# Kernel optimization log

Measured on AMD Instinct MI355X. Metric: run time of the kernel, lower is better.

The kernel has to match this reference:

```python
import jax, jax.numpy as jnp
import numpy as np

N = 100000
E = 3200000
NUM_FEATURES = 32
SEQ_LEN = 12


def setup_inputs() -> dict:
    key = jax.random.key(0)
    ks = jax.random.split(key, 32)
    x = jax.random.normal(ks[0], (N, NUM_FEATURES), dtype=jnp.float32)
    edge_index = jax.random.randint(ks[1], (2, E), 0, N, dtype=jnp.int64)

    def lin(k, fan_in, fan_out):
        k1, k2 = jax.random.split(k)
        s = 1.0 / np.sqrt(fan_in)
        W = jax.random.uniform(k1, (fan_in, fan_out), jnp.float32, -s, s)
        b = jax.random.uniform(k2, (fan_out,), jnp.float32, -s, s)
        return W, b

    W_fp, b_fp = lin(ks[2], NUM_FEATURES, 64)   # feature_proj
    W1, b1 = lin(ks[3], 64, 64)                 # conv1
    W2, b2 = lin(ks[4], 64, 32)                 # conv2
    W3, b3 = lin(ks[5], 32, 16)                 # conv3
    W_tp, b_tp = lin(ks[6], 1, 16)              # temporal_proj

    def lstm_params(k, in_dim, hid):
        k1, k2, k3, k4 = jax.random.split(k, 4)
        s = 1.0 / np.sqrt(hid)
        Wih = jax.random.uniform(k1, (4 * hid, in_dim), jnp.float32, -s, s)
        Whh = jax.random.uniform(k2, (4 * hid, hid), jnp.float32, -s, s)
        bih = jax.random.uniform(k3, (4 * hid,), jnp.float32, -s, s)
        bhh = jax.random.uniform(k4, (4 * hid,), jnp.float32, -s, s)
        return Wih, Whh, bih, bhh

    Wih0, Whh0, bih0, bhh0 = lstm_params(ks[7], 16, 32)
    Wih1, Whh1, bih1, bhh1 = lstm_params(ks[8], 32, 32)
    W_fc1, b_fc1 = lin(ks[9], 32, 16)
    W_fc2, b_fc2 = lin(ks[10], 16, 1)

    return dict(x=x, edge_index=edge_index,
                W_fp=W_fp, b_fp=b_fp, W1=W1, b1=b1, W2=W2, b2=b2, W3=W3, b3=b3,
                W_tp=W_tp, b_tp=b_tp,
                Wih0=Wih0, Whh0=Whh0, bih0=bih0, bhh0=bhh0,
                Wih1=Wih1, Whh1=Whh1, bih1=bih1, bhh1=bhh1,
                W_fc1=W_fc1, b_fc1=b_fc1, W_fc2=W_fc2, b_fc2=b_fc2)


def _gcn_conv(h, W, b, src, dst, norm, n_nodes):
    # PyG GCNConv: transform then D^-1/2 (A+I) D^-1/2 aggregation, bias after
    h = h @ W                                   # [N, out]
    msg = h[src] * norm[:, None]                # gather + scale  [E+N, out]
    out = jax.ops.segment_sum(msg, dst, num_segments=n_nodes)
    return out + b


def _lstm_layer(x_tnd, Wih, Whh, bih, bhh):
    # x_tnd: [T, N, in]; PyTorch gate order i, f, g, o
    n, hid = x_tnd.shape[1], Whh.shape[1]
    h0 = jnp.zeros((n, hid), x_tnd.dtype)
    c0 = jnp.zeros((n, hid), x_tnd.dtype)
    pre_x = jnp.einsum('tnd,gd->tng', x_tnd, Wih) + (bih + bhh)

    def step(carry, px):
        h, c = carry
        g = px + h @ Whh.T
        i, f, gg, o = jnp.split(g, 4, axis=-1)
        i = jax.nn.sigmoid(i); f = jax.nn.sigmoid(f)
        gg = jnp.tanh(gg); o = jax.nn.sigmoid(o)
        c = f * c + i * gg
        h = o * jnp.tanh(c)
        return (h, c), h

    (_, _), hs = jax.lax.scan(step, (h0, c0), pre_x)
    return hs  # [T, N, hid]


def reference(x, edge_index, W_fp, b_fp, W1, b1, W2, b2, W3, b3, W_tp, b_tp,
              Wih0, Whh0, bih0, bhh0, Wih1, Whh1, bih1, bhh1,
              W_fc1, b_fc1, W_fc2, b_fc2):
    n_nodes = x.shape[0]
    # edge filtering is a no-op here (all indices in [0, N)); add self-loops
    loops = jnp.arange(n_nodes, dtype=edge_index.dtype)
    src = jnp.concatenate([edge_index[0], loops])
    dst = jnp.concatenate([edge_index[1], loops])
    deg = jax.ops.segment_sum(jnp.ones_like(dst, dtype=x.dtype), dst,
                              num_segments=n_nodes)
    dinv = jnp.where(deg > 0, jax.lax.rsqrt(deg), 0.0)
    norm = dinv[src] * dinv[dst]

    h = jax.nn.relu(x @ W_fp + b_fp)
    h = jax.nn.relu(_gcn_conv(h, W1, b1, src, dst, norm, n_nodes))
    h = jax.nn.relu(_gcn_conv(h, W2, b2, src, dst, norm, n_nodes))
    h = jax.nn.relu(_gcn_conv(h, W3, b3, src, dst, norm, n_nodes))
    # NOTE: per the original forward, h (GCN output) is discarded below.
    _ = h

    temporal = x[:, -SEQ_LEN:].reshape(n_nodes, SEQ_LEN, 1)
    temporal = temporal @ W_tp + b_tp                 # [N, T, 16]
    t = jnp.transpose(temporal, (1, 0, 2))            # [T, N, 16]
    t = _lstm_layer(t, Wih0, Whh0, bih0, bhh0)
    t = _lstm_layer(t, Wih1, Whh1, bih1, bhh1)
    last = t[-1]                                      # [N, 32]
    out = jax.nn.relu(last @ W_fc1 + b_fc1) @ W_fc2 + b_fc2
    return out
```

## Files before the change

### kernel.cpp

```cpp
#include <hip/hip_runtime.h>

#define NN   100000
#define SEQ  12
#define NPB  48
#define XSTR 64
#define RSTR 384
#define GRID ((NN + NPB - 1) / NPB)

typedef float f32x4 __attribute__((ext_vector_type(4)));
typedef short s16x8 __attribute__((ext_vector_type(8)));

#define OFF_U    0
#define OFF_V    2048
#define OFF_B1F  4096
#define OFF_FC1  6144
#define OFF_BFC1 6656
#define OFF_FC2  6672
#define OFF_BFC2 6688
#define OFF_A    6720

#define L2E  1.4426950408889634f
#define L2E2 2.8853900817779268f

#if defined(__has_builtin)
#if __has_builtin(__builtin_amdgcn_exp2f)
#define EXP2(x) __builtin_amdgcn_exp2f(x)
#endif
#endif
#ifndef EXP2
#define EXP2(x) exp2f(x)
#endif

__device__ __forceinline__ float rcp_fast(float v) { return __builtin_amdgcn_rcpf(v); }
__device__ __forceinline__ float sigm_p(float a) { return rcp_fast(1.0f + EXP2(a)); }
__device__ __forceinline__ float tanh_p(float a) {
    return fmaf(-2.0f, rcp_fast(1.0f + EXP2(a)), 1.0f);
}
__device__ __forceinline__ unsigned short f2bf(float f) {
    unsigned u = __float_as_uint(f);
    u = u + 0x7FFFu + ((u >> 16) & 1u);
    return (unsigned short)(u >> 16);
}
__device__ __forceinline__ float bf2f(unsigned short h) {
    return __uint_as_float(((unsigned)h) << 16);
}
__device__ __forceinline__ void hsplit(float h, unsigned& uh, unsigned& ul) {
    asm("v_cvt_pk_bf16_f32 %0, %1, %1" : "=v"(uh) : "v"(h));
    const float lo = h - __uint_as_float(uh << 16);
    asm("v_cvt_pk_bf16_f32 %0, %1, %1" : "=v"(ul) : "v"(lo));
}

#define MF(a, b, c) __builtin_amdgcn_mfma_f32_16x16x32_bf16((a), (b), (c), 0, 0, 0)

__global__ void repack(const float* __restrict__ Wtp,  const float* __restrict__ btp,
                       const float* __restrict__ Wih0, const float* __restrict__ Whh0,
                       const float* __restrict__ bih0, const float* __restrict__ bhh0,
                       const float* __restrict__ Wih1, const float* __restrict__ Whh1,
                       const float* __restrict__ bih1, const float* __restrict__ bhh1,
                       const float* __restrict__ Wfc1, const float* __restrict__ bfc1,
                       const float* __restrict__ Wfc2, const float* __restrict__ bfc2,
                       float* __restrict__ ws)
{
    const int tid = threadIdx.x;
    for (int idx = tid; idx < 2048; idx += 256) {
        int tau = idx >> 8, lane = (idx >> 2) & 63, reg = idx & 3;
        int grow = 16 * tau + (lane >> 4) * 4 + reg;
        int k = grow >> 2, g = grow & 3;
        int orig = g * 32 + k;
        float sg = (g == 2) ? L2E2 : -L2E;
        float u = 0.f, v = 0.f;
        for (int d = 0; d < 16; ++d) {
            u = fmaf(Wih0[orig * 16 + d], Wtp[d], u);
            v = fmaf(Wih0[orig * 16 + d], btp[d], v);
        }
        ws[OFF_U + idx]   = sg * u;
        ws[OFF_V + idx]   = sg * (v + bih0[orig] + bhh0[orig]);
        ws[OFF_B1F + idx] = sg * (bih1[orig] + bhh1[orig]);
    }
    short* wsS = (short*)(ws + OFF_A);
    for (int idx = tid; idx < 8192; idx += 256) {
        int tau = idx >> 10, t = (idx >> 9) & 1, lane = (idx >> 3) & 63, e = idx & 7;
        int rl = lane & 15, g = rl & 3;
        int orig = g * 32 + 4 * tau + (rl >> 2);
        int j = (lane >> 4) * 8 + e;
        float sg = (g == 2) ? L2E2 : -L2E;
        float f = sg * Whh0[orig * 32 + j];
        unsigned short hi = f2bf(f);
        wsS[idx] = (short)(t == 0 ? hi : f2bf(f - bf2f(hi)));
    }
    for (int idx = tid; idx < 16384; idx += 256) {
        int tau = idx >> 11, kap = (idx >> 10) & 1, t = (idx >> 9) & 1;
        int lane = (idx >> 3) & 63, e = idx & 7;
        int rl = lane & 15, g = rl & 3;
        int orig = g * 32 + 4 * tau + (rl >> 2);
        int j = (lane >> 4) * 8 + e;
        float sg = (g == 2) ? L2E2 : -L2E;
        float f = sg * (kap ? Whh1[orig * 32 + j] : Wih1[orig * 32 + j]);
        unsigned short hi = f2bf(f);
        wsS[8192 + idx] = (short)(t == 0 ? hi : f2bf(f - bf2f(hi)));
    }
    for (int idx = tid; idx < 512; idx += 256) {
        int m = idx >> 5, j = idx & 31;
        ws[OFF_FC1 + idx] = Wfc1[j * 16 + m];
    }
    if (tid < 16) { ws[OFF_BFC1 + tid] = bfc1[tid]; ws[OFF_FC2 + tid] = Wfc2[tid]; }
    if (tid == 0) ws[OFF_BFC2] = bfc2[0];
}

template<int P>
__device__ __forceinline__ void lstm_step(
    short* __restrict__ B0, short* __restrict__ B1,
    const float*& sxp, float* __restrict__ fin,
    f32x4 uf, f32x4 vf, f32x4 b1f,
    s16x8 A0h, s16x8 A0l, s16x8 A10h, s16x8 A10l, s16x8 A11h, s16x8 A11l,
    float (&c0)[3], float (&c1)[3],
    int col, int lg, int ku, bool last)
{
    constexpr int NP = P ^ 1;
    const int nb = col * 8;
    const short* rb0 = B0 + lg * RSTR + nb;
    const short* rb1 = B1 + lg * RSTR + nb;
    short* wb0 = B0 + (ku >> 3) * RSTR + nb + (ku & 7);
    short* wb1 = B1 + (ku >> 3) * RSTR + nb + (ku & 7);

#pragma unroll
    for (int i = 0; i < 3; ++i) {
        const float xv = sxp[i * 16];
        f32x4 acc = { fmaf(uf[0], xv, vf[0]), fmaf(uf[1], xv, vf[1]),
                      fmaf(uf[2], xv, vf[2]), fmaf(uf[3], xv, vf[3]) };
        const s16x8 bh = *(const s16x8*)(rb0 + (P * 8) * RSTR + i * 128);
        const s16x8 bl = *(const s16x8*)(rb0 + (P * 8 + 4) * RSTR + i * 128);
        acc = MF(A0h, bh, acc);
        acc = MF(A0l, bh, acc);
        acc = MF(A0h, bl, acc);
        const float gi = sigm_p(acc[0]);
        const float gf = sigm_p(acc[1]);
        const float gg = tanh_p(acc[2]);
        const float go = sigm_p(acc[3]);
        const float cc = fmaf(gf, c0[i], gi * gg);
        c0[i] = cc;
        const float h = go * tanh_p(L2E2 * cc);
        unsigned uh, ul; hsplit(h, uh, ul);
        wb0[(NP * 8) * RSTR + i * 128]     = (short)uh;
        wb0[(NP * 8 + 4) * RSTR + i * 128] = (short)ul;
    }
    __syncthreads();

#pragma unroll
    for (int i = 0; i < 3; ++i) {
        f32x4 acc = { b1f[0], b1f[1], b1f[2], b1f[3] };
        const s16x8 b0h = *(const s16x8*)(rb0 + (NP * 8) * RSTR + i * 128);
        const s16x8 b0l = *(const s16x8*)(rb0 + (NP * 8 + 4) * RSTR + i * 128);
        const s16x8 b1h = *(const s16x8*)(rb1 + (P * 8) * RSTR + i * 128);
        const s16x8 b1l = *(const s16x8*)(rb1 + (P * 8 + 4) * RSTR + i * 128);
        acc = MF(A10h, b0h, acc);
        acc = MF(A10l, b0h, acc);
        acc = MF(A10h, b0l, acc);
        acc = MF(A11h, b1h, acc);
        acc = MF(A11l, b1h, acc);
        acc = MF(A11h, b1l, acc);
        const float gi = sigm_p(acc[0]);
        const float gf = sigm_p(acc[1]);
        const float gg = tanh_p(acc[2]);
        const float go = sigm_p(acc[3]);
        const float cc = fmaf(gf, c1[i], gi * gg);
        c1[i] = cc;
        const float h = go * tanh_p(L2E2 * cc);
        if (last) {
            fin[ku * NPB + col + i * 16] = h;
        } else {
            unsigned uh, ul; hsplit(h, uh, ul);
            wb1[(NP * 8) * RSTR + i * 128]     = (short)uh;
            wb1[(NP * 8 + 4) * RSTR + i * 128] = (short)ul;
        }
    }
    sxp += XSTR;
}

__global__ __launch_bounds__(512)
void lstm_mfma(const float* __restrict__ x, const float* __restrict__ ws,
               float* __restrict__ out)
{
    __shared__ short sB[2 * 16 * RSTR];
    __shared__ float sx[SEQ][XSTR];

    const int tid  = threadIdx.x;
    const int lane = tid & 63;
    const int w    = __builtin_amdgcn_readfirstlane(tid >> 6);
    const int lg   = lane >> 4, col = lane & 15;
    const int ku   = 4 * w + lg;
    const int b0   = blockIdx.x * NPB;

    for (int i = tid; i < SEQ * XSTR; i += 512) {
        int t = i >> 6, nd = i & (XSTR - 1);
        int n = b0 + nd;
        sx[t][nd] = (nd < NPB && n < NN) ? x[(size_t)n * 32 + 20 + t] : 0.f;
    }
    int* z = (int*)sB;
    for (int i = tid; i < 16 * RSTR; i += 512) z[i] = 0;

    const f32x4 uf  = *(const f32x4*)(ws + OFF_U   + (w * 64 + lane) * 4);
    const f32x4 vf  = *(const f32x4*)(ws + OFF_V   + (w * 64 + lane) * 4);
    const f32x4 b1f = *(const f32x4*)(ws + OFF_B1F + (w * 64 + lane) * 4);
    const short* AS  = (const short*)(ws + OFF_A);
    const s16x8 A0h  = *(const s16x8*)(AS + ((w * 2 + 0) * 64 + lane) * 8);
    const s16x8 A0l  = *(const s16x8*)(AS + ((w * 2 + 1) * 64 + lane) * 8);
    const short* AS1 = AS + 8192;
    const s16x8 A10h = *(const s16x8*)(AS1 + ((w * 4 + 0) * 64 + lane) * 8);
    const s16x8 A10l = *(const s16x8*)(AS1 + ((w * 4 + 1) * 64 + lane) * 8);
    const s16x8 A11h = *(const s16x8*)(AS1 + ((w * 4 + 2) * 64 + lane) * 8);
    const s16x8 A11l = *(const s16x8*)(AS1 + ((w * 4 + 3) * 64 + lane) * 8);

    short* B0 = sB;
    short* B1 = sB + 16 * RSTR;
    float* fin = (float*)(B0 + 8 * RSTR);

    float c0[3], c1[3];
#pragma unroll
    for (int i = 0; i < 3; ++i) { c0[i] = 0.f; c1[i] = 0.f; }

    __syncthreads();

    const float* sxp = &sx[0][0] + col;
#pragma unroll 1
    for (int tt = 0; tt < SEQ / 2; ++tt) {
        lstm_step<0>(B0, B1, sxp, fin, uf, vf, b1f,
                     A0h, A0l, A10h, A10l, A11h, A11l,
                     c0, c1, col, lg, ku, false);
        lstm_step<1>(B0, B1, sxp, fin, uf, vf, b1f,
                     A0h, A0l, A10h, A10l, A11h, A11l,
                     c0, c1, col, lg, ku, tt == SEQ / 2 - 1);
    }

    __syncthreads();

    if (w == 0 && lane < NPB) {
        const int nd = lane;
        float acc2 = ws[OFF_BFC2];
#pragma unroll
        for (int m = 0; m < 16; ++m) {
            const float* fp = ws + OFF_FC1 + m * 32;
            float y = ws[OFF_BFC1 + m];
#pragma unroll
            for (int j = 0; j < 32; ++j)
                y = fmaf(fp[j], fin[j * NPB + nd], y);
            acc2 = fmaf(fmaxf(y, 0.f), ws[OFF_FC2 + m], acc2);
        }
        if (b0 + nd < NN) out[b0 + nd] = acc2;
    }
}

extern "C" void kernel_launch(void* const* d_in, const int* in_sizes, int n_in,
                              void* d_out, int out_size, void* d_ws, size_t ws_size,
                              hipStream_t stream) {
    (void)in_sizes; (void)n_in; (void)out_size; (void)ws_size;
    const float* x    = (const float*)d_in[0];
    const float* Wtp  = (const float*)d_in[10];
    const float* btp  = (const float*)d_in[11];
    const float* Wih0 = (const float*)d_in[12];
    const float* Whh0 = (const float*)d_in[13];
    const float* bih0 = (const float*)d_in[14];
    const float* bhh0 = (const float*)d_in[15];
    const float* Wih1 = (const float*)d_in[16];
    const float* Whh1 = (const float*)d_in[17];
    const float* bih1 = (const float*)d_in[18];
    const float* bhh1 = (const float*)d_in[19];
    const float* Wfc1 = (const float*)d_in[20];
    const float* bfc1 = (const float*)d_in[21];
    const float* Wfc2 = (const float*)d_in[22];
    const float* bfc2 = (const float*)d_in[23];
    float* ws  = (float*)d_ws;
    float* out = (float*)d_out;

    hipLaunchKernelGGL(repack, dim3(1), dim3(256), 0, stream,
                       Wtp, btp, Wih0, Whh0, bih0, bhh0,
                       Wih1, Whh1, bih1, bhh1, Wfc1, bfc1, Wfc2, bfc2, ws);
    hipLaunchKernelGGL(lstm_mfma, dim3(GRID), dim3(512), 0, stream,
                       x, ws, out);
}
```

Measured before the change: 141.2 us.

## Halve block to 4 waves, each wave computing two gate tiles

Each block now runs 256 threads instead of 512. Every wave handles two of the eight 16-unit hidden tiles, so it holds two sets of weight fragments, biases and cell states in registers. The layer-1 MFMAs for the two tiles are interleaved so the shared B-fragment loads are reused. This targets lower barrier cost, more instruction-level parallelism per wave and fewer redundant LDS B loads, at the cost of higher register pressure and fewer waves per block to hide latency.

```diff
diff --git a/kernel.cpp b/kernel.cpp
--- a/kernel.cpp
+++ b/kernel.cpp
@@ -111,73 +111,95 @@
 __device__ __forceinline__ void lstm_step(
     short* __restrict__ B0, short* __restrict__ B1,
     const float*& sxp, float* __restrict__ fin,
-    f32x4 uf, f32x4 vf, f32x4 b1f,
-    s16x8 A0h, s16x8 A0l, s16x8 A10h, s16x8 A10l, s16x8 A11h, s16x8 A11l,
-    float (&c0)[3], float (&c1)[3],
-    int col, int lg, int ku, bool last)
+    const f32x4 (&uf)[2], const f32x4 (&vf)[2], const f32x4 (&b1f)[2],
+    const s16x8 (&A0h)[2], const s16x8 (&A0l)[2],
+    const s16x8 (&A10h)[2], const s16x8 (&A10l)[2],
+    const s16x8 (&A11h)[2], const s16x8 (&A11l)[2],
+    float (&c0)[2][3], float (&c1)[2][3],
+    int col, int lg, const int (&ku)[2], bool last)
 {
     constexpr int NP = P ^ 1;
     const int nb = col * 8;
     const short* rb0 = B0 + lg * RSTR + nb;
     const short* rb1 = B1 + lg * RSTR + nb;
-    short* wb0 = B0 + (ku >> 3) * RSTR + nb + (ku & 7);
-    short* wb1 = B1 + (ku >> 3) * RSTR + nb + (ku & 7);
 
 #pragma unroll
     for (int i = 0; i < 3; ++i) {
         const float xv = sxp[i * 16];
-        f32x4 acc = { fmaf(uf[0], xv, vf[0]), fmaf(uf[1], xv, vf[1]),
-                      fmaf(uf[2], xv, vf[2]), fmaf(uf[3], xv, vf[3]) };
         const s16x8 bh = *(const s16x8*)(rb0 + (P * 8) * RSTR + i * 128);
         const s16x8 bl = *(const s16x8*)(rb0 + (P * 8 + 4) * RSTR + i * 128);
-        acc = MF(A0h, bh, acc);
-        acc = MF(A0l, bh, acc);
-        acc = MF(A0h, bl, acc);
-        const float gi = sigm_p(acc[0]);
-        const float gf = sigm_p(acc[1]);
-        const float gg = tanh_p(acc[2]);
-        const float go = sigm_p(acc[3]);
-        const float cc = fmaf(gf, c0[i], gi * gg);
-        c0[i] = cc;
-        const float h = go * tanh_p(L2E2 * cc);
-        unsigned uh, ul; hsplit(h, uh, ul);
-        wb0[(NP * 8) * RSTR + i * 128]     = (short)uh;
-        wb0[(NP * 8 + 4) * RSTR + i * 128] = (short)ul;
+#pragma unroll
+        for (int tq = 0; tq < 2; ++tq) {
+            f32x4 acc = { fmaf(uf[tq][0], xv, vf[tq][0]),
+                          fmaf(uf[tq][1], xv, vf[tq][1]),
+                          fmaf(uf[tq][2], xv, vf[tq][2]),
+                          fmaf(uf[tq][3], xv, vf[tq][3]) };
+            acc = MF(A0h[tq], bh, acc);
+            acc = MF(A0l[tq], bh, acc);
+            acc = MF(A0h[tq], bl, acc);
+            const float gi = sigm_p(acc[0]);
+            const float gf = sigm_p(acc[1]);
+            const float gg = tanh_p(acc[2]);
+            const float go = sigm_p(acc[3]);
+            const float cc = fmaf(gf, c0[tq][i], gi * gg);
+            c0[tq][i] = cc;
+            const float h = go * tanh_p(L2E2 * cc);
+            unsigned uh, ul; hsplit(h, uh, ul);
+            short* wb = B0 + (ku[tq] >> 3) * RSTR + nb + (ku[tq] & 7);
+            wb[(NP * 8) * RSTR + i * 128]     = (short)uh;
+            wb[(NP * 8 + 4) * RSTR + i * 128] = (short)ul;
+        }
     }
     __syncthreads();
 
 #pragma unroll
     for (int i = 0; i < 3; ++i) {
-        f32x4 acc = { b1f[0], b1f[1], b1f[2], b1f[3] };
-        const s16x8 b0h = *(const s16x8*)(rb0 + (NP * 8) * RSTR + i * 128);
-        const s16x8 b0l = *(const s16x8*)(rb0 + (NP * 8 + 4) * RSTR + i * 128);
-        const s16x8 b1h = *(const s16x8*)(rb1 + (P * 8) * RSTR + i * 128);
-        const s16x8 b1l = *(const s16x8*)(rb1 + (P * 8 + 4) * RSTR + i * 128);
-        acc = MF(A10h, b0h, acc);
-        acc = MF(A10l, b0h, acc);
-        acc = MF(A10h, b0l, acc);
-        acc = MF(A11h, b1h, acc);
-        acc = MF(A11l, b1h, acc);
-        acc = MF(A11h, b1l, acc);
-        const float gi = sigm_p(acc[0]);
-        const float gf = sigm_p(acc[1]);
-        const float gg = tanh_p(acc[2]);
-        const float go = sigm_p(acc[3]);
-        const float cc = fmaf(gf, c1[i], gi * gg);
-        c1[i] = cc;
-        const float h = go * tanh_p(L2E2 * cc);
-        if (last) {
-            fin[ku * NPB + col + i * 16] = h;
-        } else {
-            unsigned uh, ul; hsplit(h, uh, ul);
-            wb1[(NP * 8) * RSTR + i * 128]     = (short)uh;
-            wb1[(NP * 8 + 4) * RSTR + i * 128] = (short)ul;
+        f32x4 acc0 = { b1f[0][0], b1f[0][1], b1f[0][2], b1f[0][3] };
+        f32x4 acc1 = { b1f[1][0], b1f[1][1], b1f[1][2], b1f[1][3] };
+        {
+            const s16x8 b0h = *(const s16x8*)(rb0 + (NP * 8) * RSTR + i * 128);
+            const s16x8 b0l = *(const s16x8*)(rb0 + (NP * 8 + 4) * RSTR + i * 128);
+            acc0 = MF(A10h[0], b0h, acc0);
+            acc1 = MF(A10h[1], b0h, acc1);
+            acc0 = MF(A10l[0], b0h, acc0);
+            acc1 = MF(A10l[1], b0h, acc1);
+            acc0 = MF(A10h[0], b0l, acc0);
+            acc1 = MF(A10h[1], b0l, acc1);
+        }
+        {
+            const s16x8 b1h = *(const s16x8*)(rb1 + (P * 8) * RSTR + i * 128);
+            const s16x8 b1l = *(const s16x8*)(rb1 + (P * 8 + 4) * RSTR + i * 128);
+            acc0 = MF(A11h[0], b1h, acc0);
+            acc1 = MF(A11h[1], b1h, acc1);
+            acc0 = MF(A11l[0], b1h, acc0);
+            acc1 = MF(A11l[1], b1h, acc1);
+            acc0 = MF(A11h[0], b1l, acc0);
+            acc1 = MF(A11h[1], b1l, acc1);
+        }
+#pragma unroll
+        for (int tq = 0; tq < 2; ++tq) {
+            const f32x4 acc = tq ? acc1 : acc0;
+            const float gi = sigm_p(acc[0]);
+            const float gf = sigm_p(acc[1]);
+            const float gg = tanh_p(acc[2]);
+            const float go = sigm_p(acc[3]);
+            const float cc = fmaf(gf, c1[tq][i], gi * gg);
+            c1[tq][i] = cc;
+            const float h = go * tanh_p(L2E2 * cc);
+            if (last) {
+                fin[ku[tq] * NPB + col + i * 16] = h;
+            } else {
+                unsigned uh, ul; hsplit(h, uh, ul);
+                short* wb = B1 + (ku[tq] >> 3) * RSTR + nb + (ku[tq] & 7);
+                wb[(NP * 8) * RSTR + i * 128]     = (short)uh;
+                wb[(NP * 8 + 4) * RSTR + i * 128] = (short)ul;
+            }
         }
     }
     sxp += XSTR;
 }
 
-__global__ __launch_bounds__(512)
+__global__ __launch_bounds__(256)
 void lstm_mfma(const float* __restrict__ x, const float* __restrict__ ws,
                float* __restrict__ out)
 {
@@ -188,36 +210,44 @@
     const int lane = tid & 63;
     const int w    = __builtin_amdgcn_readfirstlane(tid >> 6);
     const int lg   = lane >> 4, col = lane & 15;
-    const int ku   = 4 * w + lg;
     const int b0   = blockIdx.x * NPB;
-
-    for (int i = tid; i < SEQ * XSTR; i += 512) {
+    const int ku[2] = { 8 * w + lg, 8 * w + 4 + lg };
+
+    for (int i = tid; i < SEQ * XSTR; i += 256) {
         int t = i >> 6, nd = i & (XSTR - 1);
         int n = b0 + nd;
         sx[t][nd] = (nd < NPB && n < NN) ? x[(size_t)n * 32 + 20 + t] : 0.f;
     }
     int* z = (int*)sB;
-    for (int i = tid; i < 16 * RSTR; i += 512) z[i] = 0;
-
-    const f32x4 uf  = *(const f32x4*)(ws + OFF_U   + (w * 64 + lane) * 4);
-    const f32x4 vf  = *(const f32x4*)(ws + OFF_V   + (w * 64 + lane) * 4);
-    const f32x4 b1f = *(const f32x4*)(ws + OFF_B1F + (w * 64 + lane) * 4);
+    for (int i = tid; i < 16 * RSTR; i += 256) z[i] = 0;
+
+    f32x4 uf[2], vf[2], b1f[2];
+    s16x8 A0h[2], A0l[2], A10h[2], A10l[2], A11h[2], A11l[2];
     const short* AS  = (const short*)(ws + OFF_A);
-    const s16x8 A0h  = *(const s16x8*)(AS + ((w * 2 + 0) * 64 + lane) * 8);
-    const s16x8 A0l  = *(const s16x8*)(AS + ((w * 2 + 1) * 64 + lane) * 8);
     const short* AS1 = AS + 8192;
-    const s16x8 A10h = *(const s16x8*)(AS1 + ((w * 4 + 0) * 64 + lane) * 8);
-    const s16x8 A10l = *(const s16x8*)(AS1 + ((w * 4 + 1) * 64 + lane) * 8);
-    const s16x8 A11h = *(const s16x8*)(AS1 + ((w * 4 + 2) * 64 + lane) * 8);
-    const s16x8 A11l = *(const s16x8*)(AS1 + ((w * 4 + 3) * 64 + lane) * 8);
+#pragma unroll
+    for (int tq = 0; tq < 2; ++tq) {
+        const int tau = 2 * w + tq;
+        uf[tq]  = *(const f32x4*)(ws + OFF_U   + (tau * 64 + lane) * 4);
+        vf[tq]  = *(const f32x4*)(ws + OFF_V   + (tau * 64 + lane) * 4);
+        b1f[tq] = *(const f32x4*)(ws + OFF_B1F + (tau * 64 + lane) * 4);
+        A0h[tq]  = *(const s16x8*)(AS  + ((tau * 2 + 0) * 64 + lane) * 8);
+        A0l[tq]  = *(const s16x8*)(AS  + ((tau * 2 + 1) * 64 + lane) * 8);
+        A10h[tq] = *(const s16x8*)(AS1 + ((tau * 4 + 0) * 64 + lane) * 8);
+        A10l[tq] = *(const s16x8*)(AS1 + ((tau * 4 + 1) * 64 + lane) * 8);
+        A11h[tq] = *(const s16x8*)(AS1 + ((tau * 4 + 2) * 64 + lane) * 8);
+        A11l[tq] = *(const s16x8*)(AS1 + ((tau * 4 + 3) * 64 + lane) * 8);
+    }
 
     short* B0 = sB;
     short* B1 = sB + 16 * RSTR;
     float* fin = (float*)(B0 + 8 * RSTR);
 
-    float c0[3], c1[3];
-#pragma unroll
-    for (int i = 0; i < 3; ++i) { c0[i] = 0.f; c1[i] = 0.f; }
+    float c0[2][3], c1[2][3];
+#pragma unroll
+    for (int tq = 0; tq < 2; ++tq)
+#pragma unroll
+        for (int i = 0; i < 3; ++i) { c0[tq][i] = 0.f; c1[tq][i] = 0.f; }
 
     __syncthreads();
 
@@ -275,6 +305,6 @@
     hipLaunchKernelGGL(repack, dim3(1), dim3(256), 0, stream,
                        Wtp, btp, Wih0, Whh0, bih0, bhh0,
                        Wih1, Whh1, bih1, bhh1, Wfc1, bfc1, Wfc2, bfc2, ws);
-    hipLaunchKernelGGL(lstm_mfma, dim3(GRID), dim3(512), 0, stream,
+    hipLaunchKernelGGL(lstm_mfma, dim3(GRID), dim3(256), 0, stream,
                        x, ws, out);
 }
```

Result: slower. 156.5 us (+10.9%).
